# Kernel tuning notes

Measured on AMD Instinct MI355X. Metric: run time of the kernel, lower is better.

## Reference

```python
import jax, jax.numpy as jnp
import numpy as np

B, H, W = 8, 56, 56
DIM_IN = 1792 + 2   # concatenated pyramid channels + 2 coord channels
D_OUT = 1792 // 4   # gamma_d = 4
N_CENTERS = H * W   # gamma_c = 1
K = 3


def avg_pool3(x):
    # F.avg_pool2d(x, 3, 1, 1) with count_include_pad=True: padded sum / 9
    s = jax.lax.reduce_window(x, 0.0, jax.lax.add, (1, 1, 3, 3), (1, 1, 1, 1),
                              ((0, 0), (0, 0), (1, 1), (1, 1)))
    return s / 9.0


def setup_inputs() -> dict:
    key = jax.random.key(0)
    k0, k1, k2, kw, kb, kc = jax.random.split(key, 6)
    p0 = jax.random.normal(k0, (B, 256, H, W), dtype=jnp.float32)
    p1 = jax.random.normal(k1, (B, 512, 28, 28), dtype=jnp.float32)
    p2 = jax.random.normal(k2, (B, 1024, 14, 14), dtype=jnp.float32)
    conv_w = jax.random.normal(kw, (D_OUT, DIM_IN), dtype=jnp.float32) * 0.02
    conv_b = jax.random.normal(kb, (D_OUT,), dtype=jnp.float32) * 0.01
    C = jax.random.normal(kc, (D_OUT, N_CENTERS), dtype=jnp.float32) * 0.5
    return {"p0": p0, "p1": p1, "p2": p2, "conv_w": conv_w, "conv_b": conv_b, "C": C}


def reference(p0, p1, p2, conv_w, conv_b, C):
    # Descriptor: avg-pool each level, upsample to first level, concat channels
    o0 = avg_pool3(p0)
    o1 = avg_pool3(p1)
    o2 = avg_pool3(p2)
    o1 = jax.image.resize(o1, (B, o1.shape[1], H, W), method='bilinear')  # align_corners=False equiv (upsample)
    o2 = jax.image.resize(o2, (B, o2.shape[1], H, W), method='bilinear')
    sample = jnp.concatenate([o0, o1, o2], axis=1)  # (B, 1792, H, W)

    # AddCoords: xx = row index / (H-1), yy = col index / (W-1), both *2-1
    xx = (jnp.arange(H, dtype=jnp.float32) / (H - 1) * 2 - 1)[:, None] * jnp.ones((1, W), jnp.float32)
    yy = (jnp.arange(W, dtype=jnp.float32) / (W - 1) * 2 - 1)[None, :] * jnp.ones((H, 1), jnp.float32)
    coords = jnp.broadcast_to(jnp.stack([xx, yy])[None], (B, 2, H, W))
    sample = jnp.concatenate([sample, coords], axis=1)  # (B, 1794, H, W)

    # 1x1 CoordConv
    phi = jnp.einsum('bchw,oc->bohw', sample, conv_w) + conv_b[None, :, None, None]
    phi_p = phi.transpose(0, 2, 3, 1).reshape(B, H * W, D_OUT)  # b (h w) c

    # squared distance to center bank via norm expansion
    feat2 = jnp.sum(phi_p ** 2, axis=2, keepdims=True)        # (B, HW, 1)
    cent2 = jnp.sum(C ** 2, axis=0)[None, None, :]            # (1, 1, N)
    dist = jnp.sqrt(feat2 + cent2 - 2.0 * jnp.matmul(phi_p, C))  # (B, HW, N)

    # top-K smallest, ascending
    neg_top, _ = jax.lax.top_k(-dist, K)
    topv = -neg_top                                           # (B, HW, K) ascending
    soft = jax.nn.softmax(-topv, axis=-1)                     # softmin
    score = soft[:, :, 0] * topv[:, :, 0]                     # (B, HW)
    return score.reshape(B, 1, H, W)
```

## Files before the change

### kernel.cpp

```cpp
#include <hip/hip_runtime.h>
#include <math.h>

#define B_    8
#define H_    56
#define W_    56
#define HW_   3136
#define C0_   256
#define C1_   512
#define C2_   1024
#define DIN_  1794
#define KD_   1792
#define KCP_  56
#define DOUT_ 448
#define NCHP_ 28
#define NC_   3136
#define NCHD_ 196
#define KCD_  14
#define DTS_  452
#define PCH_  28672

typedef __attribute__((ext_vector_type(8))) short bh8;
typedef __attribute__((ext_vector_type(4))) float f32x4;

__device__ __forceinline__ short f2bf(float f) {
  union { float f; unsigned u; } v; v.f = f;
  unsigned r = v.u + 0x7fffu + ((v.u >> 16) & 1u);
  return (short)(r >> 16);
}
__device__ __forceinline__ float bf2f(short s) {
  union { unsigned u; float f; } v; v.u = ((unsigned)(unsigned short)s) << 16;
  return v.f;
}

__global__ __launch_bounds__(256) void desc0_kernel(const float* __restrict__ p0,
                                                    short* __restrict__ desc) {
  __shared__ float sv[64 * 57];
  const int c0 = blockIdx.x * 64, h = blockIdx.y, b = blockIdx.z;
  for (int item = threadIdx.x; item < 64 * 56; item += 256) {
    int x = item % 56, c = item / 56;
    const float* src = p0 + (((size_t)(b * C0_ + c0 + c)) * 56 + h) * 56 + x;
    float s = src[0];
    if (h > 0)  s += src[-56];
    if (h < 55) s += src[56];
    sv[c * 57 + x] = s;
  }
  __syncthreads();
  for (int item = threadIdx.x; item < 56 * 8; item += 256) {
    int g = item & 7, w = item >> 3;
    bh8 o;
#pragma unroll
    for (int j = 0; j < 8; ++j) {
      const float* s0 = sv + (g * 8 + j) * 57;
      float v = s0[w];
      if (w > 0)  v += s0[w - 1];
      if (w < 55) v += s0[w + 1];
      o[j] = f2bf(v * (1.0f / 9.0f));
    }
    size_t pid = (size_t)b * HW_ + h * 56 + w;
    *(bh8*)(desc + pid * KD_ + c0 + g * 8) = o;
  }
}

__global__ __launch_bounds__(256) void desc1_kernel(const float* __restrict__ p1,
                                                    short* __restrict__ desc) {
  __shared__ float sv[2 * 64 * 29];
  const int c0 = blockIdx.x * 64, h = blockIdx.y, b = blockIdx.z;
  float sy = (h + 0.5f) * 0.5f - 0.5f;
  float fyf = floorf(sy);
  float fy = sy - fyf;
  int iy = (int)fyf;
  int pya = min(max(iy, 0), 27), pyb = min(max(iy + 1, 0), 27);
  for (int item = threadIdx.x; item < 64 * 2 * 28; item += 256) {
    int x = item % 28;
    int pr = (item / 28) & 1;
    int c = item / 56;
    int r = pr ? pyb : pya;
    const float* src = p1 + (((size_t)(b * C1_ + c0 + c)) * 28 + r) * 28 + x;
    float s = src[0];
    if (r > 0)  s += src[-28];
    if (r < 27) s += src[28];
    sv[pr * (64 * 29) + c * 29 + x] = s;
  }
  __syncthreads();
  for (int item = threadIdx.x; item < 56 * 8; item += 256) {
    int g = item & 7, w = item >> 3;
    float sx = (w + 0.5f) * 0.5f - 0.5f;
    float fxf = floorf(sx);
    float fx = sx - fxf;
    int ix = (int)fxf;
    int x0 = min(max(ix, 0), 27), x1 = min(max(ix + 1, 0), 27);
    bh8 o;
#pragma unroll
    for (int j = 0; j < 8; ++j) {
      const float* s0 = sv + (g * 8 + j) * 29;
      const float* s1 = s0 + 64 * 29;
      float p00 = s0[x0] + (x0 > 0 ? s0[x0 - 1] : 0.f) + (x0 < 27 ? s0[x0 + 1] : 0.f);
      float p01 = s0[x1] + (x1 > 0 ? s0[x1 - 1] : 0.f) + (x1 < 27 ? s0[x1 + 1] : 0.f);
      float p10 = s1[x0] + (x0 > 0 ? s1[x0 - 1] : 0.f) + (x0 < 27 ? s1[x0 + 1] : 0.f);
      float p11 = s1[x1] + (x1 > 0 ? s1[x1 - 1] : 0.f) + (x1 < 27 ? s1[x1 + 1] : 0.f);
      float top = p00 + fx * (p01 - p00);
      float bot = p10 + fx * (p11 - p10);
      o[j] = f2bf((top + fy * (bot - top)) * (1.0f / 9.0f));
    }
    size_t pid = (size_t)b * HW_ + h * 56 + w;
    *(bh8*)(desc + pid * KD_ + C0_ + c0 + g * 8) = o;
  }
}

__global__ __launch_bounds__(256) void desc2_kernel(const float* __restrict__ p2,
                                                    short* __restrict__ desc) {
  __shared__ float sv[2 * 64 * 15];
  const int c0 = blockIdx.x * 64, h = blockIdx.y, b = blockIdx.z;
  float sy = (h + 0.5f) * 0.25f - 0.5f;
  float fyf = floorf(sy);
  float fy = sy - fyf;
  int iy = (int)fyf;
  int pya = min(max(iy, 0), 13), pyb = min(max(iy + 1, 0), 13);
  for (int item = threadIdx.x; item < 64 * 2 * 14; item += 256) {
    int x = item % 14;
    int pr = (item / 14) & 1;
    int c = item / 28;
    int r = pr ? pyb : pya;
    const float* src = p2 + (((size_t)(b * C2_ + c0 + c)) * 14 + r) * 14 + x;
    float s = src[0];
    if (r > 0)  s += src[-14];
    if (r < 13) s += src[14];
    sv[pr * (64 * 15) + c * 15 + x] = s;
  }
  __syncthreads();
  for (int item = threadIdx.x; item < 56 * 8; item += 256) {
    int g = item & 7, w = item >> 3;
    float sx = (w + 0.5f) * 0.25f - 0.5f;
    float fxf = floorf(sx);
    float fx = sx - fxf;
    int ix = (int)fxf;
    int x0 = min(max(ix, 0), 13), x1 = min(max(ix + 1, 0), 13);
    bh8 o;
#pragma unroll
    for (int j = 0; j < 8; ++j) {
      const float* s0 = sv + (g * 8 + j) * 15;
      const float* s1 = s0 + 64 * 15;
      float p00 = s0[x0] + (x0 > 0 ? s0[x0 - 1] : 0.f) + (x0 < 13 ? s0[x0 + 1] : 0.f);
      float p01 = s0[x1] + (x1 > 0 ? s0[x1 - 1] : 0.f) + (x1 < 13 ? s0[x1 + 1] : 0.f);
      float p10 = s1[x0] + (x0 > 0 ? s1[x0 - 1] : 0.f) + (x0 < 13 ? s1[x0 + 1] : 0.f);
      float p11 = s1[x1] + (x1 > 0 ? s1[x1 - 1] : 0.f) + (x1 < 13 ? s1[x1 + 1] : 0.f);
      float top = p00 + fx * (p01 - p00);
      float bot = p10 + fx * (p11 - p10);
      o[j] = f2bf((top + fy * (bot - top)) * (1.0f / 9.0f));
    }
    size_t pid = (size_t)b * HW_ + h * 56 + w;
    *(bh8*)(desc + pid * KD_ + C0_ + C1_ + c0 + g * 8) = o;
  }
}

__global__ void cent2_kernel(const float* __restrict__ C, float* __restrict__ c2) {
  int j = blockIdx.x * blockDim.x + threadIdx.x;
  if (j >= NC_) return;
  float s = 0.f;
  for (int d = 0; d < DOUT_; ++d) {
    float v = bf2f(f2bf(C[(size_t)d * NC_ + j]));
    s = fmaf(v, v, s);
  }
  c2[j] = s;
}

__global__ void cpack_kernel(const float* __restrict__ C, short* __restrict__ Cpk) {
  int idx = blockIdx.x * 256 + threadIdx.x;
  int ln = idx & 63;
  int kc = (idx >> 6) % KCD_;
  int nc = idx / (KCD_ * 64);
  int n  = nc * 16 + (ln & 15);
  int k0 = kc * 32 + ((ln >> 4) << 3);
  bh8 o;
#pragma unroll
  for (int j = 0; j < 8; ++j) o[j] = f2bf(C[(size_t)(k0 + j) * NC_ + n]);
  *(bh8*)(Cpk + (size_t)idx * 8) = o;
}

__global__ void wpack_kernel(const float* __restrict__ W, short* __restrict__ Wpk) {
  int idx = blockIdx.x * 256 + threadIdx.x;
  int ln = idx & 63;
  int kc = (idx >> 6) % KCP_;
  int nc = idx / (KCP_ * 64);
  int n  = nc * 16 + (ln & 15);
  int k0 = kc * 32 + ((ln >> 4) << 3);
  bh8 o;
#pragma unroll
  for (int j = 0; j < 8; ++j) o[j] = f2bf(W[(size_t)n * DIN_ + k0 + j]);
  *(bh8*)(Wpk + (size_t)idx * 8) = o;
}

__global__ __launch_bounds__(256) void phi_mfma(
    const short* __restrict__ desc, const short* __restrict__ Wpk,
    const float* __restrict__ cw, const float* __restrict__ cb,
    short* __restrict__ phip ) {
  __shared__ __align__(16) float Dt[16 * DTS_];
  const int wv = threadIdx.x >> 6, ln = threadIdx.x & 63;
  const int pix0 = blockIdx.x * 32;
  const short* aptr = desc + ((size_t)(pix0 + (ln & 15))) * KD_ + ((ln >> 4) << 3);

  f32x4 acc[2][7];
#pragma unroll
  for (int rc = 0; rc < 2; ++rc)
#pragma unroll
    for (int i = 0; i < 7; ++i) acc[rc][i] = (f32x4){0.f, 0.f, 0.f, 0.f};

  const short* bbase = Wpk + (size_t)(wv * 7) * (KCP_ * 512) + ln * 8;
  for (int kc = 0; kc < KCP_; ++kc) {
    bh8 a0 = *(const bh8*)(aptr + kc * 32);
    bh8 a1 = *(const bh8*)(aptr + 16 * KD_ + kc * 32);
    const short* bp = bbase + kc * 512;
#pragma unroll
    for (int i = 0; i < 7; ++i) {
      bh8 bfr = *(const bh8*)(bp + (size_t)i * (KCP_ * 512));
      acc[0][i] = __builtin_amdgcn_mfma_f32_16x16x32_bf16(a0, bfr, acc[0][i], 0, 0, 0);
      acc[1][i] = __builtin_amdgcn_mfma_f32_16x16x32_bf16(a1, bfr, acc[1][i], 0, 0, 0);
    }
  }

  for (int rc = 0; rc < 2; ++rc) {
    __syncthreads();
#pragma unroll
    for (int i = 0; i < 7; ++i) {
      int col = (wv * 7 + i) * 16 + (ln & 15);
      float bias = cb[col];
      float wx = cw[(size_t)col * DIN_ + 1792];
      float wy = cw[(size_t)col * DIN_ + 1793];
#pragma unroll
      for (int r = 0; r < 4; ++r) {
        int row = ((ln >> 4) << 2) + r;
        int pid = pix0 + rc * 16 + row;
        int hw = pid % HW_;
        int hh = hw / 56, ww = hw % 56;
        float xx = (float)hh * (2.0f / 55.0f) - 1.0f;
        float yy = (float)ww * (2.0f / 55.0f) - 1.0f;
        Dt[row * DTS_ + col] = acc[rc][i][r] + bias + wx * xx + wy * yy;
      }
    }
    __syncthreads();
    short* op = phip + (size_t)(blockIdx.x * 2 + rc) * PCH_;
    for (int item = threadIdx.x; item < KCD_ * 64; item += 256) {
      int kc = item >> 6, lp = item & 63;
      int m = lp & 15, k0 = kc * 32 + ((lp >> 4) << 3);
      bh8 o;
#pragma unroll
      for (int j = 0; j < 8; ++j) o[j] = f2bf(Dt[m * DTS_ + k0 + j]);
      *(bh8*)(op + (size_t)item * 8) = o;
    }
  }
}

__device__ __forceinline__ void insert3(float& t0, float& t1, float& t2, float v) {
  if (v < t2) {
    if (v < t1) {
      t2 = t1;
      if (v < t0) { t1 = t0; t0 = v; } else t1 = v;
    } else t2 = v;
  }
}
__device__ __forceinline__ void merge3(float& a0, float& a1, float& a2,
                                       float b0, float b1, float b2) {
  float lo0 = fminf(a0, b0), hi0 = fmaxf(a0, b0);
  float lo1 = fminf(a1, b1), hi1 = fmaxf(a1, b1);
  float lo2 = fminf(a2, b2);
  a0 = lo0;
  a1 = fminf(hi0, lo1);
  a2 = fminf(fmaxf(hi0, lo1), fminf(hi1, lo2));
}
__device__ __forceinline__ float sumsq8(bh8 a, float s) {
#pragma unroll
  for (int j = 0; j < 8; ++j) { float v = bf2f(a[j]); s = fmaf(v, v, s); }
  return s;
}

#define AFRAG_LIST(X) X(0) X(1) X(2) X(3) X(4) X(5) X(6) X(7) X(8) X(9) X(10) X(11) X(12) X(13)

__global__ __launch_bounds__(256, 4) void dist_part(
    const short* __restrict__ phip, const short* __restrict__ Cpk,
    const float* __restrict__ c2g, float* __restrict__ part) {
  const int wv = threadIdx.x >> 6, ln = threadIdx.x & 63;
  const int chunk = blockIdx.x * 2 + (wv >> 1);
  const int half  = wv & 1;

  const short* ap = phip + (size_t)chunk * PCH_ + ln * 8;
#define LOADA(i) bh8 A##i = *(const bh8*)(ap + (i) * 512);
  AFRAG_LIST(LOADA)
#undef LOADA

  float sum = 0.f;
#define SQ(i) sum = sumsq8(A##i, sum);
  AFRAG_LIST(SQ)
#undef SQ
  sum += __shfl_xor(sum, 16, 64);
  sum += __shfl_xor(sum, 32, 64);
  const int rb = (ln >> 4) << 2;
  float f2r0 = __shfl(sum, rb + 0, 64);
  float f2r1 = __shfl(sum, rb + 1, 64);
  float f2r2 = __shfl(sum, rb + 2, 64);
  float f2r3 = __shfl(sum, rb + 3, 64);

  float t00 = 1e30f, t01 = 1e30f, t02 = 1e30f;
  float t10 = 1e30f, t11 = 1e30f, t12 = 1e30f;
  float t20 = 1e30f, t21 = 1e30f, t22 = 1e30f;
  float t30 = 1e30f, t31 = 1e30f, t32 = 1e30f;

  const int nc0 = half * (NCHD_ / 2);
  const short* bbase = Cpk + (size_t)nc0 * (KCD_ * 512) + ln * 8;
  const float* c2base = c2g + (size_t)nc0 * 16 + (ln & 15);
  for (int i = 0; i < NCHD_ / 4; ++i) {
    const short* bpA = bbase + (size_t)(2 * i) * (KCD_ * 512);
    const short* bpB = bpA + (KCD_ * 512);
    f32x4 accA = {0.f, 0.f, 0.f, 0.f}, accB = {0.f, 0.f, 0.f, 0.f};
#define MF(kc) { \
    bh8 bA = *(const bh8*)(bpA + (kc) * 512); \
    bh8 bB = *(const bh8*)(bpB + (kc) * 512); \
    accA = __builtin_amdgcn_mfma_f32_16x16x32_bf16(A##kc, bA, accA, 0, 0, 0); \
    accB = __builtin_amdgcn_mfma_f32_16x16x32_bf16(A##kc, bB, accB, 0, 0, 0); }
    AFRAG_LIST(MF)
#undef MF
    float c2A = c2base[(size_t)(2 * i) * 16];
    float c2B = c2base[(size_t)(2 * i + 1) * 16];
    insert3(t00, t01, t02, f2r0 + c2A - 2.0f * accA[0]);
    insert3(t10, t11, t12, f2r1 + c2A - 2.0f * accA[1]);
    insert3(t20, t21, t22, f2r2 + c2A - 2.0f * accA[2]);
    insert3(t30, t31, t32, f2r3 + c2A - 2.0f * accA[3]);
    insert3(t00, t01, t02, f2r0 + c2B - 2.0f * accB[0]);
    insert3(t10, t11, t12, f2r1 + c2B - 2.0f * accB[1]);
    insert3(t20, t21, t22, f2r2 + c2B - 2.0f * accB[2]);
    insert3(t30, t31, t32, f2r3 + c2B - 2.0f * accB[3]);
  }

#pragma unroll
  for (int m = 1; m <= 8; m <<= 1) {
    float b0, b1, b2;
    b0 = __shfl_xor(t00, m, 64); b1 = __shfl_xor(t01, m, 64); b2 = __shfl_xor(t02, m, 64);
    merge3(t00, t01, t02, b0, b1, b2);
    b0 = __shfl_xor(t10, m, 64); b1 = __shfl_xor(t11, m, 64); b2 = __shfl_xor(t12, m, 64);
    merge3(t10, t11, t12, b0, b1, b2);
    b0 = __shfl_xor(t20, m, 64); b1 = __shfl_xor(t21, m, 64); b2 = __shfl_xor(t22, m, 64);
    merge3(t20, t21, t22, b0, b1, b2);
    b0 = __shfl_xor(t30, m, 64); b1 = __shfl_xor(t31, m, 64); b2 = __shfl_xor(t32, m, 64);
    merge3(t30, t31, t32, b0, b1, b2);
  }

  if ((ln & 15) == 0) {
    float* q = part + ((size_t)(chunk * 16 + rb)) * 8 + half * 4;
    q[0] = t00; q[1] = t01; q[2] = t02;
    q[8] = t10; q[9] = t11; q[10] = t12;
    q[16] = t20; q[17] = t21; q[18] = t22;
    q[24] = t30; q[25] = t31; q[26] = t32;
  }
}

__global__ __launch_bounds__(256) void merge_kernel(const float* __restrict__ part,
                                                    float* __restrict__ out) {
  int p = blockIdx.x * 256 + threadIdx.x;
  const float* q = part + (size_t)p * 8;
  float a0 = q[0], a1 = q[1], a2 = q[2];
  merge3(a0, a1, a2, q[4], q[5], q[6]);
  float d0 = sqrtf(fmaxf(a0, 0.f));
  float d1 = sqrtf(fmaxf(a1, 0.f));
  float d2 = sqrtf(fmaxf(a2, 0.f));
  float s0 = 1.0f / (1.0f + expf(d0 - d1) + expf(d0 - d2));
  out[p] = s0 * d0;
}

extern "C" void kernel_launch(void* const* d_in, const int* in_sizes, int n_in,
                              void* d_out, int out_size, void* d_ws, size_t ws_size,
                              hipStream_t stream) {
  const float* p0 = (const float*)d_in[0];
  const float* p1 = (const float*)d_in[1];
  const float* p2 = (const float*)d_in[2];
  const float* cw = (const float*)d_in[3];
  const float* cb = (const float*)d_in[4];
  const float* C  = (const float*)d_in[5];
  float* out = (float*)d_out;

  short* desc = (short*)d_ws;
  short* Cpk  = desc + (size_t)25088 * KD_;
  short* Wpk  = Cpk + (size_t)NCHD_ * KCD_ * 512;
  float* c2   = (float*)(Wpk + (size_t)NCHP_ * KCP_ * 512);
  float* part = c2 + NC_;

  desc0_kernel<<<dim3(4, 56, 8),  256, 0, stream>>>(p0, desc);
  desc1_kernel<<<dim3(8, 56, 8),  256, 0, stream>>>(p1, desc);
  desc2_kernel<<<dim3(16, 56, 8), 256, 0, stream>>>(p2, desc);
  cent2_kernel<<<(NC_ + 255) / 256, 256, 0, stream>>>(C, c2);
  cpack_kernel<<<NCHD_ * KCD_ * 64 / 256, 256, 0, stream>>>(C, Cpk);
  wpack_kernel<<<NCHP_ * KCP_ * 64 / 256, 256, 0, stream>>>(cw, Wpk);
  phi_mfma<<<25088 / 32, 256, 0, stream>>>(desc, Wpk, cw, cb, desc);
  dist_part<<<25088 / 32, 256, 0, stream>>>(desc, Cpk, c2, part);
  merge_kernel<<<25088 / 256, 256, 0, stream>>>(part, out);
}
```

Measured before the change: 682.2 us.

## Stage center bank tiles in LDS with double-buffered async loads in dist_part

Reorganizes dist_part so each block's four waves share one half of the center bank. Center tiles are staged into double-buffered shared memory with global_load_lds, and the center norms are cached in LDS. Previously each wave streamed its own B fragments from global memory, so four waves now reuse each staged tile instead of each fetching it. The cost is a block-wide barrier per iteration, about 70KB of LDS per block, and occupancy lowered to 2 blocks per CU.

```diff
diff --git a/kernel.cpp b/kernel.cpp
--- a/kernel.cpp
+++ b/kernel.cpp
@@ -275,12 +275,16 @@
 
 #define AFRAG_LIST(X) X(0) X(1) X(2) X(3) X(4) X(5) X(6) X(7) X(8) X(9) X(10) X(11) X(12) X(13)
 
-__global__ __launch_bounds__(256, 4) void dist_part(
+__global__ __launch_bounds__(256, 2) void dist_part(
     const short* __restrict__ phip, const short* __restrict__ Cpk,
     const float* __restrict__ c2g, float* __restrict__ part) {
+  __shared__ __align__(16) short Bst[2][14336];
+  __shared__ float c2l[NC_ / 2];
   const int wv = threadIdx.x >> 6, ln = threadIdx.x & 63;
-  const int chunk = blockIdx.x * 2 + (wv >> 1);
-  const int half  = wv & 1;
+  const int half = blockIdx.x & 1;
+  const int chunk = (blockIdx.x >> 1) * 4 + wv;
+
+  for (int i = threadIdx.x; i < NC_ / 2; i += 256) c2l[i] = c2g[half * (NC_ / 2) + i];
 
   const short* ap = phip + (size_t)chunk * PCH_ + ln * 8;
 #define LOADA(i) bh8 A##i = *(const bh8*)(ap + (i) * 512);
@@ -304,22 +308,35 @@
   float t20 = 1e30f, t21 = 1e30f, t22 = 1e30f;
   float t30 = 1e30f, t31 = 1e30f, t32 = 1e30f;
 
-  const int nc0 = half * (NCHD_ / 2);
-  const short* bbase = Cpk + (size_t)nc0 * (KCD_ * 512) + ln * 8;
-  const float* c2base = c2g + (size_t)nc0 * 16 + (ln & 15);
-  for (int i = 0; i < NCHD_ / 4; ++i) {
-    const short* bpA = bbase + (size_t)(2 * i) * (KCD_ * 512);
-    const short* bpB = bpA + (KCD_ * 512);
+  const int col = ln & 15;
+  const short* cbase = Cpk + (size_t)half * ((NCHD_ / 2) * KCD_ * 512);
+
+#define STAGE(buf, t) { \
+    const short* g_ = cbase + (size_t)(t) * 14336 + wv * 3584 + ln * 8; \
+    short* l_ = &Bst[(buf)][wv * 3584]; \
+    _Pragma("unroll") \
+    for (int j_ = 0; j_ < 7; ++j_) \
+      __builtin_amdgcn_global_load_lds( \
+          (const __attribute__((address_space(1))) unsigned int*)(g_ + j_ * 512), \
+          (__attribute__((address_space(3))) unsigned int*)(l_ + j_ * 512), \
+          16, 0, 0); }
+
+  STAGE(0, 0)
+  __syncthreads();
+
+  for (int t = 0; t < NCHD_ / 4; ++t) {
+    if (t < NCHD_ / 4 - 1) STAGE((t + 1) & 1, t + 1)
+    const short* bp = &Bst[t & 1][ln * 8];
     f32x4 accA = {0.f, 0.f, 0.f, 0.f}, accB = {0.f, 0.f, 0.f, 0.f};
 #define MF(kc) { \
-    bh8 bA = *(const bh8*)(bpA + (kc) * 512); \
-    bh8 bB = *(const bh8*)(bpB + (kc) * 512); \
+    bh8 bA = *(const bh8*)(bp + (kc) * 512); \
+    bh8 bB = *(const bh8*)(bp + 7168 + (kc) * 512); \
     accA = __builtin_amdgcn_mfma_f32_16x16x32_bf16(A##kc, bA, accA, 0, 0, 0); \
     accB = __builtin_amdgcn_mfma_f32_16x16x32_bf16(A##kc, bB, accB, 0, 0, 0); }
     AFRAG_LIST(MF)
 #undef MF
-    float c2A = c2base[(size_t)(2 * i) * 16];
-    float c2B = c2base[(size_t)(2 * i + 1) * 16];
+    float c2A = c2l[t * 32 + col];
+    float c2B = c2l[t * 32 + 16 + col];
     insert3(t00, t01, t02, f2r0 + c2A - 2.0f * accA[0]);
     insert3(t10, t11, t12, f2r1 + c2A - 2.0f * accA[1]);
     insert3(t20, t21, t22, f2r2 + c2A - 2.0f * accA[2]);
@@ -328,7 +345,9 @@
     insert3(t10, t11, t12, f2r1 + c2B - 2.0f * accB[1]);
     insert3(t20, t21, t22, f2r2 + c2B - 2.0f * accB[2]);
     insert3(t30, t31, t32, f2r3 + c2B - 2.0f * accB[3]);
-  }
+    __syncthreads();
+  }
+#undef STAGE
 
 #pragma unroll
   for (int m = 1; m <= 8; m <<= 1) {
@@ -389,6 +408,6 @@
   cpack_kernel<<<NCHD_ * KCD_ * 64 / 256, 256, 0, stream>>>(C, Cpk);
   wpack_kernel<<<NCHP_ * KCP_ * 64 / 256, 256, 0, stream>>>(cw, Wpk);
   phi_mfma<<<25088 / 32, 256, 0, stream>>>(desc, Wpk, cw, cb, desc);
-  dist_part<<<25088 / 32, 256, 0, stream>>>(desc, Cpk, c2, part);
+  dist_part<<<784, 256, 0, stream>>>(desc, Cpk, c2, part);
   merge_kernel<<<25088 / 256, 256, 0, stream>>>(part, out);
 }
```

New measurement: 721.8 us. +5.8%, slower.

## Software-pipeline operand loads in phi and distance MFMA loops

Applied to the files above, without the earlier changes.

The phi GEMM loop is restructured into a double-buffered schedule: A and B fragments for the next k-chunks are loaded into registers while MFMAs run on the current ones, with sched_barrier fences keeping the order. The distance kernel likewise prefetches the next center chunk's B fragments and c2 value during the current chunk's MFMAs, handling one center chunk per iteration instead of two interleaved ones. Its occupancy hint drops from 4 to 3 blocks per SM to make room for the extra prefetch registers. The aim is to hide global load latency behind matrix math, at the cost of higher register pressure, lower occupancy, and a single serial accumulator chain in the distance loop.

```diff
diff --git a/kernel.cpp b/kernel.cpp
--- a/kernel.cpp
+++ b/kernel.cpp
@@ -190,6 +190,8 @@
   *(bh8*)(Wpk + (size_t)idx * 8) = o;
 }
 
+#define L7(X) X(0) X(1) X(2) X(3) X(4) X(5) X(6)
+
 __global__ __launch_bounds__(256) void phi_mfma(
     const short* __restrict__ desc, const short* __restrict__ Wpk,
     const float* __restrict__ cw, const float* __restrict__ cb,
@@ -198,6 +200,7 @@
   const int wv = threadIdx.x >> 6, ln = threadIdx.x & 63;
   const int pix0 = blockIdx.x * 32;
   const short* aptr = desc + ((size_t)(pix0 + (ln & 15))) * KD_ + ((ln >> 4) << 3);
+  const short* bbase = Wpk + (size_t)(wv * 7) * (KCP_ * 512) + ln * 8;
 
   f32x4 acc[2][7];
 #pragma unroll
@@ -205,18 +208,43 @@
 #pragma unroll
     for (int i = 0; i < 7; ++i) acc[rc][i] = (f32x4){0.f, 0.f, 0.f, 0.f};
 
-  const short* bbase = Wpk + (size_t)(wv * 7) * (KCP_ * 512) + ln * 8;
-  for (int kc = 0; kc < KCP_; ++kc) {
-    bh8 a0 = *(const bh8*)(aptr + kc * 32);
-    bh8 a1 = *(const bh8*)(aptr + 16 * KD_ + kc * 32);
-    const short* bp = bbase + kc * 512;
-#pragma unroll
-    for (int i = 0; i < 7; ++i) {
-      bh8 bfr = *(const bh8*)(bp + (size_t)i * (KCP_ * 512));
-      acc[0][i] = __builtin_amdgcn_mfma_f32_16x16x32_bf16(a0, bfr, acc[0][i], 0, 0, 0);
-      acc[1][i] = __builtin_amdgcn_mfma_f32_16x16x32_bf16(a1, bfr, acc[1][i], 0, 0, 0);
-    }
-  }
+#define WOFF(i, kc) ((size_t)(i) * (KCP_ * 512) + (size_t)(kc) * 512)
+  bh8 xa0 = *(const bh8*)(aptr);
+  bh8 xa1 = *(const bh8*)(aptr + 16 * KD_);
+#define PX(i) bh8 xb##i = *(const bh8*)(bbase + WOFF(i, 0));
+  L7(PX)
+#undef PX
+  bh8 ya0 = *(const bh8*)(aptr + 32);
+  bh8 ya1 = *(const bh8*)(aptr + 16 * KD_ + 32);
+#define PY(i) bh8 yb##i = *(const bh8*)(bbase + WOFF(i, 1));
+  L7(PY)
+#undef PY
+
+  for (int it = 0; it < 28; ++it) {
+    int kc2 = 2 * it + 2; if (kc2 >= 56) kc2 = 0;
+    int kc3 = 2 * it + 3; if (kc3 >= 56) kc3 = 1;
+#define CX(i) acc[0][i] = __builtin_amdgcn_mfma_f32_16x16x32_bf16(xa0, xb##i, acc[0][i], 0, 0, 0); \
+              acc[1][i] = __builtin_amdgcn_mfma_f32_16x16x32_bf16(xa1, xb##i, acc[1][i], 0, 0, 0);
+    L7(CX)
+#undef CX
+    xa0 = *(const bh8*)(aptr + (size_t)kc2 * 32);
+    xa1 = *(const bh8*)(aptr + 16 * KD_ + (size_t)kc2 * 32);
+#define RX(i) xb##i = *(const bh8*)(bbase + WOFF(i, kc2));
+    L7(RX)
+#undef RX
+    __builtin_amdgcn_sched_barrier(0);
+#define CY(i) acc[0][i] = __builtin_amdgcn_mfma_f32_16x16x32_bf16(ya0, yb##i, acc[0][i], 0, 0, 0); \
+              acc[1][i] = __builtin_amdgcn_mfma_f32_16x16x32_bf16(ya1, yb##i, acc[1][i], 0, 0, 0);
+    L7(CY)
+#undef CY
+    ya0 = *(const bh8*)(aptr + (size_t)kc3 * 32);
+    ya1 = *(const bh8*)(aptr + 16 * KD_ + (size_t)kc3 * 32);
+#define RY(i) yb##i = *(const bh8*)(bbase + WOFF(i, kc3));
+    L7(RY)
+#undef RY
+    __builtin_amdgcn_sched_barrier(0);
+  }
+#undef WOFF
 
   for (int rc = 0; rc < 2; ++rc) {
     __syncthreads();
@@ -275,7 +303,7 @@
 
 #define AFRAG_LIST(X) X(0) X(1) X(2) X(3) X(4) X(5) X(6) X(7) X(8) X(9) X(10) X(11) X(12) X(13)
 
-__global__ __launch_bounds__(256, 4) void dist_part(
+__global__ __launch_bounds__(256, 3) void dist_part(
     const short* __restrict__ phip, const short* __restrict__ Cpk,
     const float* __restrict__ c2g, float* __restrict__ part) {
   const int wv = threadIdx.x >> 6, ln = threadIdx.x & 63;
@@ -304,30 +332,49 @@
   float t20 = 1e30f, t21 = 1e30f, t22 = 1e30f;
   float t30 = 1e30f, t31 = 1e30f, t32 = 1e30f;
 
-  const int nc0 = half * (NCHD_ / 2);
-  const short* bbase = Cpk + (size_t)nc0 * (KCD_ * 512) + ln * 8;
-  const float* c2base = c2g + (size_t)nc0 * 16 + (ln & 15);
-  for (int i = 0; i < NCHD_ / 4; ++i) {
-    const short* bpA = bbase + (size_t)(2 * i) * (KCD_ * 512);
-    const short* bpB = bpA + (KCD_ * 512);
-    f32x4 accA = {0.f, 0.f, 0.f, 0.f}, accB = {0.f, 0.f, 0.f, 0.f};
-#define MF(kc) { \
-    bh8 bA = *(const bh8*)(bpA + (kc) * 512); \
-    bh8 bB = *(const bh8*)(bpB + (kc) * 512); \
-    accA = __builtin_amdgcn_mfma_f32_16x16x32_bf16(A##kc, bA, accA, 0, 0, 0); \
-    accB = __builtin_amdgcn_mfma_f32_16x16x32_bf16(A##kc, bB, accB, 0, 0, 0); }
-    AFRAG_LIST(MF)
-#undef MF
-    float c2A = c2base[(size_t)(2 * i) * 16];
-    float c2B = c2base[(size_t)(2 * i + 1) * 16];
-    insert3(t00, t01, t02, f2r0 + c2A - 2.0f * accA[0]);
-    insert3(t10, t11, t12, f2r1 + c2A - 2.0f * accA[1]);
-    insert3(t20, t21, t22, f2r2 + c2A - 2.0f * accA[2]);
-    insert3(t30, t31, t32, f2r3 + c2A - 2.0f * accA[3]);
-    insert3(t00, t01, t02, f2r0 + c2B - 2.0f * accB[0]);
-    insert3(t10, t11, t12, f2r1 + c2B - 2.0f * accB[1]);
-    insert3(t20, t21, t22, f2r2 + c2B - 2.0f * accB[2]);
-    insert3(t30, t31, t32, f2r3 + c2B - 2.0f * accB[3]);
+  const short* cb = Cpk + ((size_t)half * (NCHD_ / 2)) * (KCD_ * 512) + ln * 8;
+  const float* c2b = c2g + half * (NC_ / 2) + (ln & 15);
+
+#define PRP(i) bh8 P##i = *(const bh8*)(cb + (i) * 512);
+  L7(PRP)
+#undef PRP
+#define PRQ(i) bh8 Q##i = *(const bh8*)(cb + (7 + (i)) * 512);
+  L7(PRQ)
+#undef PRQ
+  float c2cur = c2b[0];
+
+  for (int nc = 0; nc < NCHD_ / 2; ++nc) {
+    int ncn = (nc < NCHD_ / 2 - 1) ? nc + 1 : nc;
+    const short* bn = cb + (size_t)ncn * (KCD_ * 512);
+    f32x4 acc = {0.f, 0.f, 0.f, 0.f};
+    acc = __builtin_amdgcn_mfma_f32_16x16x32_bf16(A0, P0, acc, 0, 0, 0);
+    acc = __builtin_amdgcn_mfma_f32_16x16x32_bf16(A1, P1, acc, 0, 0, 0);
+    acc = __builtin_amdgcn_mfma_f32_16x16x32_bf16(A2, P2, acc, 0, 0, 0);
+    acc = __builtin_amdgcn_mfma_f32_16x16x32_bf16(A3, P3, acc, 0, 0, 0);
+    acc = __builtin_amdgcn_mfma_f32_16x16x32_bf16(A4, P4, acc, 0, 0, 0);
+    acc = __builtin_amdgcn_mfma_f32_16x16x32_bf16(A5, P5, acc, 0, 0, 0);
+    acc = __builtin_amdgcn_mfma_f32_16x16x32_bf16(A6, P6, acc, 0, 0, 0);
+#define RP(i) P##i = *(const bh8*)(bn + (i) * 512);
+    L7(RP)
+#undef RP
+    __builtin_amdgcn_sched_barrier(0);
+    acc = __builtin_amdgcn_mfma_f32_16x16x32_bf16(A7,  Q0, acc, 0, 0, 0);
+    acc = __builtin_amdgcn_mfma_f32_16x16x32_bf16(A8,  Q1, acc, 0, 0, 0);
+    acc = __builtin_amdgcn_mfma_f32_16x16x32_bf16(A9,  Q2, acc, 0, 0, 0);
+    acc = __builtin_amdgcn_mfma_f32_16x16x32_bf16(A10, Q3, acc, 0, 0, 0);
+    acc = __builtin_amdgcn_mfma_f32_16x16x32_bf16(A11, Q4, acc, 0, 0, 0);
+    acc = __builtin_amdgcn_mfma_f32_16x16x32_bf16(A12, Q5, acc, 0, 0, 0);
+    acc = __builtin_amdgcn_mfma_f32_16x16x32_bf16(A13, Q6, acc, 0, 0, 0);
+#define RQ(i) Q##i = *(const bh8*)(bn + (7 + (i)) * 512);
+    L7(RQ)
+#undef RQ
+    float c2n = c2b[(size_t)ncn * 16];
+    __builtin_amdgcn_sched_barrier(0);
+    insert3(t00, t01, t02, f2r0 + c2cur - 2.0f * acc[0]);
+    insert3(t10, t11, t12, f2r1 + c2cur - 2.0f * acc[1]);
+    insert3(t20, t21, t22, f2r2 + c2cur - 2.0f * acc[2]);
+    insert3(t30, t31, t32, f2r3 + c2cur - 2.0f * acc[3]);
+    c2cur = c2n;
   }
 
 #pragma unroll
```

New measurement: 757.2 us. +11.0%, slower.

## Stage query rows in LDS and split center bank across four waves per block

Applied to the files above, without the earlier changes.

dist_part now gives each block one 16-row query chunk. The A fragments are copied into shared memory with global_load_lds, and each of the four waves scans a quarter of the center chunks, reading A from LDS instead of holding it in registers. Per-wave top-3 results are merged through a small shared array before being written out as the two halves the merge kernel expects. This frees the registers that held A for more occupancy and loads each query chunk once per block, at the cost of LDS reads on every MFMA, twice as many blocks, and one MFMA chain per iteration instead of two interleaved ones.

```diff
diff --git a/kernel.cpp b/kernel.cpp
--- a/kernel.cpp
+++ b/kernel.cpp
@@ -273,24 +273,33 @@
   return s;
 }
 
-#define AFRAG_LIST(X) X(0) X(1) X(2) X(3) X(4) X(5) X(6) X(7) X(8) X(9) X(10) X(11) X(12) X(13)
+#define KLIST(X) X(0) X(1) X(2) X(3) X(4) X(5) X(6) X(7) X(8) X(9) X(10) X(11) X(12) X(13)
 
 __global__ __launch_bounds__(256, 4) void dist_part(
     const short* __restrict__ phip, const short* __restrict__ Cpk,
     const float* __restrict__ c2g, float* __restrict__ part) {
+  __shared__ __align__(16) short Asl[14336];
+  __shared__ float tri[4][16][4];
   const int wv = threadIdx.x >> 6, ln = threadIdx.x & 63;
-  const int chunk = blockIdx.x * 2 + (wv >> 1);
-  const int half  = wv & 1;
-
-  const short* ap = phip + (size_t)chunk * PCH_ + ln * 8;
-#define LOADA(i) bh8 A##i = *(const bh8*)(ap + (i) * 512);
-  AFRAG_LIST(LOADA)
-#undef LOADA
+  const int chunk = blockIdx.x;
+
+  {
+    const short* g_ = phip + (size_t)chunk * PCH_ + wv * 3584 + ln * 8;
+    short* l_ = Asl + wv * 3584;
+#pragma unroll
+    for (int j = 0; j < 7; ++j)
+      __builtin_amdgcn_global_load_lds(
+          (const __attribute__((address_space(1))) unsigned int*)(g_ + j * 512),
+          (__attribute__((address_space(3))) unsigned int*)(l_ + j * 512),
+          16, 0, 0);
+  }
+  __syncthreads();
+
+  const short* alds = Asl + ln * 8;
 
   float sum = 0.f;
-#define SQ(i) sum = sumsq8(A##i, sum);
-  AFRAG_LIST(SQ)
-#undef SQ
+#pragma unroll
+  for (int i = 0; i < 14; ++i) sum = sumsq8(*(const bh8*)(alds + i * 512), sum);
   sum += __shfl_xor(sum, 16, 64);
   sum += __shfl_xor(sum, 32, 64);
   const int rb = (ln >> 4) << 2;
@@ -304,30 +313,24 @@
   float t20 = 1e30f, t21 = 1e30f, t22 = 1e30f;
   float t30 = 1e30f, t31 = 1e30f, t32 = 1e30f;
 
-  const int nc0 = half * (NCHD_ / 2);
-  const short* bbase = Cpk + (size_t)nc0 * (KCD_ * 512) + ln * 8;
-  const float* c2base = c2g + (size_t)nc0 * 16 + (ln & 15);
-  for (int i = 0; i < NCHD_ / 4; ++i) {
-    const short* bpA = bbase + (size_t)(2 * i) * (KCD_ * 512);
-    const short* bpB = bpA + (KCD_ * 512);
-    f32x4 accA = {0.f, 0.f, 0.f, 0.f}, accB = {0.f, 0.f, 0.f, 0.f};
-#define MF(kc) { \
-    bh8 bA = *(const bh8*)(bpA + (kc) * 512); \
-    bh8 bB = *(const bh8*)(bpB + (kc) * 512); \
-    accA = __builtin_amdgcn_mfma_f32_16x16x32_bf16(A##kc, bA, accA, 0, 0, 0); \
-    accB = __builtin_amdgcn_mfma_f32_16x16x32_bf16(A##kc, bB, accB, 0, 0, 0); }
-    AFRAG_LIST(MF)
+  const short* cb = Cpk + (size_t)wv * 49 * (KCD_ * 512) + ln * 8;
+  const float* c2b = c2g + wv * 49 * 16 + (ln & 15);
+
+  for (int nc = 0; nc < 49; ++nc) {
+    const short* bp = cb + (size_t)nc * (KCD_ * 512);
+#define LB(kc) bh8 B##kc = *(const bh8*)(bp + (kc) * 512);
+    KLIST(LB)
+#undef LB
+    f32x4 acc = {0.f, 0.f, 0.f, 0.f};
+#define MF(kc) acc = __builtin_amdgcn_mfma_f32_16x16x32_bf16( \
+        *(const bh8*)(alds + (kc) * 512), B##kc, acc, 0, 0, 0);
+    KLIST(MF)
 #undef MF
-    float c2A = c2base[(size_t)(2 * i) * 16];
-    float c2B = c2base[(size_t)(2 * i + 1) * 16];
-    insert3(t00, t01, t02, f2r0 + c2A - 2.0f * accA[0]);
-    insert3(t10, t11, t12, f2r1 + c2A - 2.0f * accA[1]);
-    insert3(t20, t21, t22, f2r2 + c2A - 2.0f * accA[2]);
-    insert3(t30, t31, t32, f2r3 + c2A - 2.0f * accA[3]);
-    insert3(t00, t01, t02, f2r0 + c2B - 2.0f * accB[0]);
-    insert3(t10, t11, t12, f2r1 + c2B - 2.0f * accB[1]);
-    insert3(t20, t21, t22, f2r2 + c2B - 2.0f * accB[2]);
-    insert3(t30, t31, t32, f2r3 + c2B - 2.0f * accB[3]);
+    float c2v = c2b[nc * 16];
+    insert3(t00, t01, t02, f2r0 + c2v - 2.0f * acc[0]);
+    insert3(t10, t11, t12, f2r1 + c2v - 2.0f * acc[1]);
+    insert3(t20, t21, t22, f2r2 + c2v - 2.0f * acc[2]);
+    insert3(t30, t31, t32, f2r3 + c2v - 2.0f * acc[3]);
   }
 
 #pragma unroll
@@ -344,11 +347,18 @@
   }
 
   if ((ln & 15) == 0) {
-    float* q = part + ((size_t)(chunk * 16 + rb)) * 8 + half * 4;
-    q[0] = t00; q[1] = t01; q[2] = t02;
-    q[8] = t10; q[9] = t11; q[10] = t12;
-    q[16] = t20; q[17] = t21; q[18] = t22;
-    q[24] = t30; q[25] = t31; q[26] = t32;
+    tri[wv][rb + 0][0] = t00; tri[wv][rb + 0][1] = t01; tri[wv][rb + 0][2] = t02;
+    tri[wv][rb + 1][0] = t10; tri[wv][rb + 1][1] = t11; tri[wv][rb + 1][2] = t12;
+    tri[wv][rb + 2][0] = t20; tri[wv][rb + 2][1] = t21; tri[wv][rb + 2][2] = t22;
+    tri[wv][rb + 3][0] = t30; tri[wv][rb + 3][1] = t31; tri[wv][rb + 3][2] = t32;
+  }
+  __syncthreads();
+  if (threadIdx.x < 32) {
+    int p = threadIdx.x & 15, hh = threadIdx.x >> 4;
+    float a0 = tri[2 * hh][p][0], a1 = tri[2 * hh][p][1], a2 = tri[2 * hh][p][2];
+    merge3(a0, a1, a2, tri[2 * hh + 1][p][0], tri[2 * hh + 1][p][1], tri[2 * hh + 1][p][2]);
+    float* o = part + ((size_t)(chunk * 16 + p)) * 8 + hh * 4;
+    o[0] = a0; o[1] = a1; o[2] = a2;
   }
 }
 
@@ -389,6 +399,6 @@
   cpack_kernel<<<NCHD_ * KCD_ * 64 / 256, 256, 0, stream>>>(C, Cpk);
   wpack_kernel<<<NCHP_ * KCP_ * 64 / 256, 256, 0, stream>>>(cw, Wpk);
   phi_mfma<<<25088 / 32, 256, 0, stream>>>(desc, Wpk, cw, cb, desc);
-  dist_part<<<25088 / 32, 256, 0, stream>>>(desc, Cpk, c2, part);
+  dist_part<<<1568, 256, 0, stream>>>(desc, Cpk, c2, part);
   merge_kernel<<<25088 / 256, 256, 0, stream>>>(part, out);
 }
```

Result: no change. 687.0 us (+0.7%).
